# Performance work log

Measured on AMD Instinct MI355X. Metric: run time of the kernel, lower is better.

Reference implementation:

```python
import jax, jax.numpy as jnp
import numpy as np
import jax.ops

N = 100000   # nodes
E = 3200000  # edges
B = 256      # graphs in batch
F_IN, H, C = 128, 64, 2


def gcn_conv(x, src, dst, W, b):
    # PyG GCNConv: x' = D^{-1/2} (A + I) D^{-1/2} (x W) + b
    n = x.shape[0]
    h = x @ W  # [N, H]
    loop = jnp.arange(n)
    s = jnp.concatenate([src, loop])  # add self-loops
    d = jnp.concatenate([dst, loop])
    deg = jax.ops.segment_sum(jnp.ones_like(d, dtype=h.dtype), d, num_segments=n)
    dinv = jnp.where(deg > 0, jax.lax.rsqrt(deg), 0.0)
    norm = dinv[s] * dinv[d]  # [E+N]
    msg = h[s] * norm[:, None]  # gather + scale
    out = jax.ops.segment_sum(msg, d, num_segments=n)  # scatter-add
    return out + b


def setup_inputs() -> dict:
    key = jax.random.key(0)
    ks = jax.random.split(key, 10)
    x = jax.random.normal(ks[0], (N, F_IN), dtype=jnp.float32)
    edge_index = jax.random.randint(ks[1], (2, E), 0, N, dtype=jnp.int64)
    batch = jnp.sort(jax.random.randint(ks[2], (N,), 0, B, dtype=jnp.int64))
    glorot = lambda k, fi, fo: jax.random.uniform(k, (fi, fo), jnp.float32, -1, 1) * np.sqrt(6.0 / (fi + fo))
    return {
        "x": x, "edge_index": edge_index, "batch": batch,
        "W1": glorot(ks[3], F_IN, H), "b1": jnp.zeros((H,), jnp.float32),
        "W2": glorot(ks[4], H, H), "b2": jnp.zeros((H,), jnp.float32),
        "Wl": glorot(ks[5], H, C), "bl": jnp.zeros((C,), jnp.float32),
    }


def reference(x, edge_index, batch, W1, b1, W2, b2, Wl, bl):
    src, dst = edge_index[0], edge_index[1]
    h = jax.nn.relu(gcn_conv(x, src, dst, W1, b1))
    h = jax.nn.relu(gcn_conv(h, src, dst, W2, b2))
    # global_mean_pool over graph ids
    sums = jax.ops.segment_sum(h, batch, num_segments=B)
    cnt = jax.ops.segment_sum(jnp.ones((h.shape[0],), h.dtype), batch, num_segments=B)
    pooled = sums / jnp.maximum(cnt, 1.0)[:, None]  # [B, H]
    return pooled @ Wl + bl  # [B, C]
```

## Files before the change

### kernel.cpp

```cpp
#include <hip/hip_runtime.h>
#include <hip/hip_bf16.h>


#define HDIM 64
#define NB 256
#define SGRID 256

typedef __attribute__((ext_vector_type(8))) short short8;
typedef __attribute__((ext_vector_type(4))) float f32x4;
union FragU { uint4 u; short8 s; };

static __device__ __forceinline__ unsigned bf16_bits(float f) {
    unsigned u = __float_as_uint(f);
    return (u + 0x7fff + ((u >> 16) & 1)) >> 16;
}
static __device__ __forceinline__ float bflo(unsigned w) { return __uint_as_float(w << 16); }
static __device__ __forceinline__ float bfhi(unsigned w) { return __uint_as_float(w & 0xffff0000u); }


__global__ __launch_bounds__(1024) void k_bcount(const int* __restrict__ dst,
        int* __restrict__ blkhist, int E, int npb, int chunk) {
    __shared__ int lh[NB];
    int tid = threadIdx.x;
    if (tid < NB) lh[tid] = 0;
    __syncthreads();
    int e0 = blockIdx.x * chunk, e1 = min(E, e0 + chunk);
    for (int e = e0 + tid; e < e1; e += 1024)
        atomicAdd(&lh[(unsigned)dst[e] / (unsigned)npb], 1);
    __syncthreads();
    if (tid < NB) blkhist[blockIdx.x * NB + tid] = lh[tid];
}

__global__ void k_bscan2(int* __restrict__ blkhist, int* __restrict__ bcnt) {
    __shared__ int s[SGRID];
    int b = blockIdx.x, t = threadIdx.x;
    int orig = blkhist[t * NB + b];
    s[t] = orig;
    __syncthreads();
    for (int off = 1; off < SGRID; off <<= 1) {
        int v = 0;
        if (t >= off) v = s[t - off];
        __syncthreads();
        s[t] += v;
        __syncthreads();
    }
    blkhist[t * NB + b] = s[t] - orig;
    if (t == SGRID - 1) bcnt[b] = s[t];
}

__global__ void k_bscan(const int* __restrict__ bcnt, int* __restrict__ bstart) {
    __shared__ int s[NB];
    int t = threadIdx.x;
    int orig = bcnt[t];
    s[t] = orig;
    __syncthreads();
    for (int off = 1; off < NB; off <<= 1) {
        int v = 0;
        if (t >= off) v = s[t - off];
        __syncthreads();
        s[t] += v;
        __syncthreads();
    }
    bstart[t] = s[t] - orig;
    if (t == NB - 1) bstart[NB] = s[t];
}

__global__ __launch_bounds__(1024) void k_bscatter(const int* __restrict__ src,
        const int* __restrict__ dst, const int* __restrict__ bstart,
        const int* __restrict__ blkhist, unsigned* __restrict__ ebuf,
        int E, int npb, int chunk) {
    __shared__ int base[NB], lcur[NB];
    int tid = threadIdx.x;
    if (tid < NB) {
        base[tid] = bstart[tid] + blkhist[blockIdx.x * NB + tid];
        lcur[tid] = 0;
    }
    __syncthreads();
    int e0 = blockIdx.x * chunk, e1 = min(E, e0 + chunk);
    for (int e = e0 + tid; e < e1; e += 1024) {
        int d = dst[e];
        unsigned b = (unsigned)d / (unsigned)npb;
        unsigned ld = (unsigned)d - b * (unsigned)npb;
        int off = atomicAdd(&lcur[b], 1);
        ebuf[base[b] + off] = (ld << 17) | (unsigned)src[e];
    }
}

__global__ __launch_bounds__(1024) void k_bfill(const unsigned* __restrict__ ebuf,
        const int* __restrict__ bstart, int* __restrict__ row_start,
        int* __restrict__ cnt8, float* __restrict__ dinv, int* __restrict__ csr,
        int N, int npb) {
    __shared__ int h[512], p[512], c[512];
    int b = blockIdx.x, tid = threadIdx.x;
    int vlo = b * npb;
    int vcnt = min(npb, N - vlo);
    if (vcnt <= 0) return;
    for (int i = tid; i < 512; i += 1024) h[i] = 0;
    __syncthreads();
    int e0 = bstart[b], e1 = bstart[b + 1];
    for (int e = e0 + tid; e < e1; e += 1024)
        atomicAdd(&h[ebuf[e] >> 17], 1);
    __syncthreads();
    int pc = 0;
    if (tid < 512) {
        pc = (tid < vcnt) ? ((h[tid] + 7) & ~7) : 0;
        p[tid] = pc;
    }
    __syncthreads();
    for (int off = 1; off < 512; off <<= 1) {
        int v = 0;
        if (tid < 512 && tid >= off) v = p[tid - off];
        __syncthreads();
        if (tid < 512) p[tid] += v;
        __syncthreads();
    }
    int bb = e0 + 7 * vlo;
    if (tid < vcnt) {
        int excl = p[tid] - pc;
        int v = vlo + tid;
        row_start[v] = bb + excl;
        cnt8[v] = pc >> 3;
        dinv[v] = rsqrtf((float)(h[tid] + 1));
        c[tid] = excl;
    }
    __syncthreads();
    for (int e = e0 + tid; e < e1; e += 1024) {
        unsigned ed = ebuf[e];
        int off = atomicAdd(&c[ed >> 17], 1);
        csr[bb + off] = (int)(ed & 0x1FFFFu);
    }
    __syncthreads();
    if (tid < vcnt) {
        int excl = p[tid] - pc;
        for (int q = excl + h[tid]; q < excl + pc; ++q) csr[bb + q] = N;
    }
}

__global__ void k_prep(const float* __restrict__ W1, const float* __restrict__ W2,
                       uint4* __restrict__ W1s, uint4* __restrict__ W2s,
                       unsigned* __restrict__ hsbA, unsigned* __restrict__ hsbB, int N) {
    int t = threadIdx.x;
    int lane = t & 63, ci = t >> 6;
    {
        int kt = ci >> 2, nt = ci & 3;
        int kbase = kt * 32 + (lane >> 4) * 8;
        int n = nt * 16 + (lane & 15);
        uint4 o;
        unsigned* op = (unsigned*)&o;
        for (int jj = 0; jj < 4; ++jj) {
            unsigned lo = bf16_bits(W1[(kbase + 2 * jj) * 64 + n]);
            unsigned hi = bf16_bits(W1[(kbase + 2 * jj + 1) * 64 + n]);
            op[jj] = lo | (hi << 16);
        }
        W1s[ci * 64 + lane] = o;
    }
    if (ci < 8) {
        int kt = ci >> 2, nt = ci & 3;
        int kbase = kt * 32 + (lane >> 4) * 8;
        int n = nt * 16 + (lane & 15);
        uint4 o;
        unsigned* op = (unsigned*)&o;
        for (int jj = 0; jj < 4; ++jj) {
            unsigned lo = bf16_bits(W2[(kbase + 2 * jj) * 64 + n]);
            unsigned hi = bf16_bits(W2[(kbase + 2 * jj + 1) * 64 + n]);
            op[jj] = lo | (hi << 16);
        }
        W2s[ci * 64 + lane] = o;
    }
    if (t < 32) hsbA[(size_t)N * 32 + t] = 0;
    else if (t < 64) hsbB[(size_t)N * 32 + (t - 32)] = 0;
}

#define MFMA_EPILOGUE(OUT)                                                     \
    {                                                                          \
        int col = lane & 15;                                                   \
        float dv[4];                                                           \
        for (int r = 0; r < 4; ++r) {                                          \
            int vr = v0 + quad * 4 + r;                                        \
            dv[r] = dinv[vr < n ? vr : (n - 1)];                               \
        }                                                                      \
        for (int nt = 0; nt < 4; ++nt)                                         \
            for (int r = 0; r < 4; ++r) {                                      \
                int vr = v0 + quad * 4 + r;                                    \
                float val = acc[nt][r] * dv[r];                                \
                float oth = __shfl_xor(val, 1, 64);                            \
                if (!(lane & 1) && vr < n)                                     \
                    OUT[(size_t)vr * 32 + nt * 8 + (col >> 1)] =               \
                        bf16_bits(val) | (bf16_bits(oth) << 16);               \
            }                                                                  \
    }

__global__ __launch_bounds__(256) void k_mgemm1(const float* __restrict__ X,
        const uint4* __restrict__ W1s, const float* __restrict__ dinv,
        unsigned* __restrict__ hsb, int n) {
    int lane = threadIdx.x & 63, wv = threadIdx.x >> 6;
    int v0 = (blockIdx.x * 4 + wv) * 16;
    if (v0 >= n) return;
    int quad = lane >> 4;
    int vm = v0 + (lane & 15); if (vm >= n) vm = n - 1;
    const float* xr = X + (size_t)vm * 128 + quad * 8;
    f32x4 acc[4] = {f32x4{0,0,0,0}, f32x4{0,0,0,0}, f32x4{0,0,0,0}, f32x4{0,0,0,0}};
#pragma unroll
    for (int kt = 0; kt < 4; ++kt) {
        float4 xa = *(const float4*)(xr + kt * 32);
        float4 xb = *(const float4*)(xr + kt * 32 + 4);
        FragU a;
        a.u.x = bf16_bits(xa.x) | (bf16_bits(xa.y) << 16);
        a.u.y = bf16_bits(xa.z) | (bf16_bits(xa.w) << 16);
        a.u.z = bf16_bits(xb.x) | (bf16_bits(xb.y) << 16);
        a.u.w = bf16_bits(xb.z) | (bf16_bits(xb.w) << 16);
#pragma unroll
        for (int nt = 0; nt < 4; ++nt) {
            FragU b; b.u = W1s[(kt * 4 + nt) * 64 + lane];
            acc[nt] = __builtin_amdgcn_mfma_f32_16x16x32_bf16(a.s, b.s, acc[nt], 0, 0, 0);
        }
    }
    MFMA_EPILOGUE(hsb)
}

__global__ __launch_bounds__(256) void k_mgemm2(const unsigned* __restrict__ h1b,
        const uint4* __restrict__ W2s, const float* __restrict__ dinv,
        unsigned* __restrict__ hsbB, int n) {
    int lane = threadIdx.x & 63, wv = threadIdx.x >> 6;
    int v0 = (blockIdx.x * 4 + wv) * 16;
    if (v0 >= n) return;
    int quad = lane >> 4;
    int vm = v0 + (lane & 15); if (vm >= n) vm = n - 1;
    const uint4* h4 = (const uint4*)h1b;
    f32x4 acc[4] = {f32x4{0,0,0,0}, f32x4{0,0,0,0}, f32x4{0,0,0,0}, f32x4{0,0,0,0}};
#pragma unroll
    for (int kt = 0; kt < 2; ++kt) {
        FragU a; a.u = h4[(size_t)vm * 8 + kt * 4 + quad];
#pragma unroll
        for (int nt = 0; nt < 4; ++nt) {
            FragU b; b.u = W2s[(kt * 4 + nt) * 64 + lane];
            acc[nt] = __builtin_amdgcn_mfma_f32_16x16x32_bf16(a.s, b.s, acc[nt], 0, 0, 0);
        }
    }
    MFMA_EPILOGUE(hsbB)
}

#define GATHER_BODY                                                            \
    const uint4* hs4p = (const uint4*)hsb;                                     \
    int o = lane & 7, oct = lane >> 3;                                         \
    float a0=0.f,a1=0.f,a2=0.f,a3=0.f,a4=0.f,a5=0.f,a6=0.f,a7=0.f;             \
    if (oct == 0) {                                                            \
        uint4 s = hs4p[(size_t)v * 8 + o];                                     \
        a0=bflo(s.x);a1=bfhi(s.x);a2=bflo(s.y);a3=bfhi(s.y);                   \
        a4=bflo(s.z);a5=bfhi(s.z);a6=bflo(s.w);a7=bfhi(s.w);                   \
    }                                                                          \
    int rs = row_start[v], nb = cnt8[v];                                       \
    for (int base = 0; base < nb; base += 8) {                                 \
        int idx = csr[rs + base * 8 + lane];   \
        int m = nb - base; if (m > 8) m = 8;                 \
        uint4 wb[8];                                                           \
        _Pragma("unroll")                                                      \
        for (int i = 0; i < 8; ++i)                                            \
            if (i < m) {                                                       \
                int u = __shfl(idx, i * 8 + oct, 64);                          \
                wb[i] = hs4p[(size_t)u * 8 + o];                               \
            }                                                                  \
        _Pragma("unroll")                                                      \
        for (int i = 0; i < 8; ++i)                                            \
            if (i < m) {                                                       \
                a0+=bflo(wb[i].x);a1+=bfhi(wb[i].x);                           \
                a2+=bflo(wb[i].y);a3+=bfhi(wb[i].y);                           \
                a4+=bflo(wb[i].z);a5+=bfhi(wb[i].z);                           \
                a6+=bflo(wb[i].w);a7+=bfhi(wb[i].w);                           \
            }                                                                  \
    }                                                                          \
    a0+=__shfl_xor(a0,8,64);a0+=__shfl_xor(a0,16,64);a0+=__shfl_xor(a0,32,64); \
    a1+=__shfl_xor(a1,8,64);a1+=__shfl_xor(a1,16,64);a1+=__shfl_xor(a1,32,64); \
    a2+=__shfl_xor(a2,8,64);a2+=__shfl_xor(a2,16,64);a2+=__shfl_xor(a2,32,64); \
    a3+=__shfl_xor(a3,8,64);a3+=__shfl_xor(a3,16,64);a3+=__shfl_xor(a3,32,64); \
    a4+=__shfl_xor(a4,8,64);a4+=__shfl_xor(a4,16,64);a4+=__shfl_xor(a4,32,64); \
    a5+=__shfl_xor(a5,8,64);a5+=__shfl_xor(a5,16,64);a5+=__shfl_xor(a5,32,64); \
    a6+=__shfl_xor(a6,8,64);a6+=__shfl_xor(a6,16,64);a6+=__shfl_xor(a6,32,64); \
    a7+=__shfl_xor(a7,8,64);a7+=__shfl_xor(a7,16,64);a7+=__shfl_xor(a7,32,64); \
    float dv = dinv[v];                                                        \
    float4 bb0 = ((const float4*)bias)[2 * o];                                 \
    float4 bb1 = ((const float4*)bias)[2 * o + 1];                             \
    float r0 = fmaxf(fmaf(dv, a0, bb0.x), 0.f);                                \
    float r1 = fmaxf(fmaf(dv, a1, bb0.y), 0.f);                                \
    float r2 = fmaxf(fmaf(dv, a2, bb0.z), 0.f);                                \
    float r3 = fmaxf(fmaf(dv, a3, bb0.w), 0.f);                                \
    float r4 = fmaxf(fmaf(dv, a4, bb1.x), 0.f);                                \
    float r5 = fmaxf(fmaf(dv, a5, bb1.y), 0.f);                                \
    float r6 = fmaxf(fmaf(dv, a6, bb1.z), 0.f);                                \
    float r7 = fmaxf(fmaf(dv, a7, bb1.w), 0.f);

__global__ void k_conv1(const unsigned* __restrict__ hsb, const int* __restrict__ row_start,
                        const int* __restrict__ cnt8, const int* __restrict__ csr,
                        const float* __restrict__ dinv, const float* __restrict__ bias,
                        unsigned* __restrict__ h1b, int n) {
    int v = (blockIdx.x * 256 + threadIdx.x) >> 6;
    int lane = threadIdx.x & 63;
    if (v >= n) return;
    GATHER_BODY
    if (oct == 0) {
        uint4 pk;
        pk.x = bf16_bits(r0) | (bf16_bits(r1) << 16);
        pk.y = bf16_bits(r2) | (bf16_bits(r3) << 16);
        pk.z = bf16_bits(r4) | (bf16_bits(r5) << 16);
        pk.w = bf16_bits(r6) | (bf16_bits(r7) << 16);
        ((uint4*)h1b)[(size_t)v * 8 + o] = pk;
    }
}

__global__ void k_conv_out(const unsigned* __restrict__ hsb, const int* __restrict__ row_start,
                           const int* __restrict__ cnt8, const int* __restrict__ csr,
                           const float* __restrict__ dinv, const float* __restrict__ bias,
                           const float* __restrict__ Wl, float2* __restrict__ z, int n) {
    int v = (blockIdx.x * 256 + threadIdx.x) >> 6;
    int lane = threadIdx.x & 63;
    if (v >= n) return;
    GATHER_BODY
    const float4* Wl4 = (const float4*)Wl;
    float4 wA = Wl4[4 * o + 0];
    float4 wB = Wl4[4 * o + 1];
    float4 wC = Wl4[4 * o + 2];
    float4 wD = Wl4[4 * o + 3];
    float c0 = r0*wA.x + r1*wA.z + r2*wB.x + r3*wB.z + r4*wC.x + r5*wC.z + r6*wD.x + r7*wD.z;
    float c1 = r0*wA.y + r1*wA.w + r2*wB.y + r3*wB.w + r4*wC.y + r5*wC.w + r6*wD.y + r7*wD.w;
    c0 += __shfl_xor(c0, 1, 64); c1 += __shfl_xor(c1, 1, 64);
    c0 += __shfl_xor(c0, 2, 64); c1 += __shfl_xor(c1, 2, 64);
    c0 += __shfl_xor(c0, 4, 64); c1 += __shfl_xor(c1, 4, 64);
    if (lane == 0) z[v] = make_float2(c0, c1);
}

static __device__ __forceinline__ int lower_bound(const int* __restrict__ a, int n, int key) {
    int lo = 0, hi = n;
    while (lo < hi) {
        int mid = (lo + hi) >> 1;
        if (a[mid] < key) lo = mid + 1; else hi = mid;
    }
    return lo;
}

__global__ void k_pool_z(const float2* __restrict__ z, const int* __restrict__ batch,
                         const float* __restrict__ bl, float* __restrict__ out, int N, int B) {
    int g = (blockIdx.x * 256 + threadIdx.x) >> 6;
    int lane = threadIdx.x & 63;
    if (g >= B) return;
    int lo = lower_bound(batch, N, g);
    int hi = lower_bound(batch, N, g + 1);
    float c0 = 0.f, c1 = 0.f;
    for (int v = lo + lane; v < hi; v += 64) {
        float2 t = z[v];
        c0 += t.x; c1 += t.y;
    }
    #pragma unroll
    for (int off = 32; off; off >>= 1) {
        c0 += __shfl_xor(c0, off, 64);
        c1 += __shfl_xor(c1, off, 64);
    }
    if (lane == 0) {
        float inv = 1.0f / fmaxf((float)(hi - lo), 1.0f);
        out[g * 2 + 0] = c0 * inv + bl[0];
        out[g * 2 + 1] = c1 * inv + bl[1];
    }
}

extern "C" void kernel_launch(void* const* d_in, const int* in_sizes, int n_in,
                              void* d_out, int out_size, void* d_ws, size_t ws_size,
                              hipStream_t stream) {
    const float* x  = (const float*)d_in[0];
    const int* edge = (const int*)d_in[1];
    const int* batch= (const int*)d_in[2];
    const float* W1 = (const float*)d_in[3];
    const float* b1 = (const float*)d_in[4];
    const float* W2 = (const float*)d_in[5];
    const float* b2 = (const float*)d_in[6];
    const float* Wl = (const float*)d_in[7];
    const float* bl = (const float*)d_in[8];
    float* out = (float*)d_out;

    const int N = in_sizes[2];
    const int E = in_sizes[1] / 2;
    const int B = out_size / 2;
    const int* srcp = edge;
    const int* dstp = edge + E;
    const int npb = (N + NB - 1) / NB;

    char* w = (char*)d_ws;
    auto carve = [&](size_t bytes) { void* p = (void*)w; w += (bytes + 255) & ~(size_t)255; return p; };
    int*      cnt8    = (int*)carve((size_t)N * 4);
    int*      rsA     = (int*)carve((size_t)N * 4);
    float*    dinv    = (float*)carve((size_t)N * 4);
    int*      bcnt    = (int*)carve((NB + 8) * 4);
    int*      bstart  = (int*)carve((NB + 8) * 4);
    int*      blkhist = (int*)carve((size_t)SGRID * NB * 4);
    uint4*    W1s     = (uint4*)carve(16 * 64 * 16);
    uint4*    W2s     = (uint4*)carve(8 * 64 * 16);
    int*      csr     = (int*)carve(((size_t)E + 7 * (size_t)N + 256) * 4);
    unsigned* hsbA    = (unsigned*)carve(((size_t)N + 1) * 32 * 4);
    unsigned* ebuf    = hsbA;
    unsigned* h1b     = (unsigned*)carve(((size_t)N + 1) * 32 * 4);
    unsigned* hsbB    = (unsigned*)carve(((size_t)N + 1) * 32 * 4);
    float2*   zbuf    = (float2*)carve((size_t)N * 8);

    const int chunk = (E + SGRID - 1) / SGRID;
    int wbl = (N + 3) / 4;
    int gbl = (N + 63) / 64;

    k_bcount<<<SGRID, 1024, 0, stream>>>(dstp, blkhist, E, npb, chunk);
    k_bscan2<<<NB, SGRID, 0, stream>>>(blkhist, bcnt);
    k_bscan<<<1, NB, 0, stream>>>(bcnt, bstart);
    k_bscatter<<<SGRID, 1024, 0, stream>>>(srcp, dstp, bstart, blkhist, ebuf, E, npb, chunk);
    k_bfill<<<NB, 1024, 0, stream>>>(ebuf, bstart, rsA, cnt8, dinv, csr, N, npb);
    k_prep<<<1, 1024, 0, stream>>>(W1, W2, W1s, W2s, hsbA, hsbB, N);

    k_mgemm1<<<gbl, 256, 0, stream>>>(x, W1s, dinv, hsbA, N);
    k_conv1<<<wbl, 256, 0, stream>>>(hsbA, rsA, cnt8, csr, dinv, b1, h1b, N);
    k_mgemm2<<<gbl, 256, 0, stream>>>(h1b, W2s, dinv, hsbB, N);
    k_conv_out<<<wbl, 256, 0, stream>>>(hsbB, rsA, cnt8, csr, dinv, b2, Wl, zbuf, N);

    k_pool_z<<<(B * 64 + 255) / 256, 256, 0, stream>>>(zbuf, batch, bl, out, N, B);
}
```

Measured before the change: 324.9 us.

## Fuse bucket scan with weight prep, stage X in LDS, restructure gather loop

```diff
diff --git a/kernel.cpp b/kernel.cpp
--- a/kernel.cpp
+++ b/kernel.cpp
@@ -8,6 +8,7 @@
 
 typedef __attribute__((ext_vector_type(8))) short short8;
 typedef __attribute__((ext_vector_type(4))) float f32x4;
+typedef __attribute__((ext_vector_type(2))) float f32x2;
 union FragU { uint4 u; short8 s; };
 
 static __device__ __forceinline__ unsigned bf16_bits(float f) {
@@ -48,98 +49,24 @@
     if (t == SGRID - 1) bcnt[b] = s[t];
 }
 
-__global__ void k_bscan(const int* __restrict__ bcnt, int* __restrict__ bstart) {
+__global__ __launch_bounds__(1024) void k_bscan_prep(const int* __restrict__ bcnt,
+        int* __restrict__ bstart, const float* __restrict__ W1,
+        const float* __restrict__ W2, uint4* __restrict__ W1s, uint4* __restrict__ W2s,
+        unsigned* __restrict__ hsbA, unsigned* __restrict__ hsbB, int N) {
     __shared__ int s[NB];
     int t = threadIdx.x;
-    int orig = bcnt[t];
-    s[t] = orig;
+    int orig = 0;
+    if (t < NB) { orig = bcnt[t]; s[t] = orig; }
     __syncthreads();
     for (int off = 1; off < NB; off <<= 1) {
         int v = 0;
-        if (t >= off) v = s[t - off];
-        __syncthreads();
-        s[t] += v;
-        __syncthreads();
-    }
-    bstart[t] = s[t] - orig;
+        if (t < NB && t >= off) v = s[t - off];
+        __syncthreads();
+        if (t < NB) s[t] += v;
+        __syncthreads();
+    }
+    if (t < NB) bstart[t] = s[t] - orig;
     if (t == NB - 1) bstart[NB] = s[t];
-}
-
-__global__ __launch_bounds__(1024) void k_bscatter(const int* __restrict__ src,
-        const int* __restrict__ dst, const int* __restrict__ bstart,
-        const int* __restrict__ blkhist, unsigned* __restrict__ ebuf,
-        int E, int npb, int chunk) {
-    __shared__ int base[NB], lcur[NB];
-    int tid = threadIdx.x;
-    if (tid < NB) {
-        base[tid] = bstart[tid] + blkhist[blockIdx.x * NB + tid];
-        lcur[tid] = 0;
-    }
-    __syncthreads();
-    int e0 = blockIdx.x * chunk, e1 = min(E, e0 + chunk);
-    for (int e = e0 + tid; e < e1; e += 1024) {
-        int d = dst[e];
-        unsigned b = (unsigned)d / (unsigned)npb;
-        unsigned ld = (unsigned)d - b * (unsigned)npb;
-        int off = atomicAdd(&lcur[b], 1);
-        ebuf[base[b] + off] = (ld << 17) | (unsigned)src[e];
-    }
-}
-
-__global__ __launch_bounds__(1024) void k_bfill(const unsigned* __restrict__ ebuf,
-        const int* __restrict__ bstart, int* __restrict__ row_start,
-        int* __restrict__ cnt8, float* __restrict__ dinv, int* __restrict__ csr,
-        int N, int npb) {
-    __shared__ int h[512], p[512], c[512];
-    int b = blockIdx.x, tid = threadIdx.x;
-    int vlo = b * npb;
-    int vcnt = min(npb, N - vlo);
-    if (vcnt <= 0) return;
-    for (int i = tid; i < 512; i += 1024) h[i] = 0;
-    __syncthreads();
-    int e0 = bstart[b], e1 = bstart[b + 1];
-    for (int e = e0 + tid; e < e1; e += 1024)
-        atomicAdd(&h[ebuf[e] >> 17], 1);
-    __syncthreads();
-    int pc = 0;
-    if (tid < 512) {
-        pc = (tid < vcnt) ? ((h[tid] + 7) & ~7) : 0;
-        p[tid] = pc;
-    }
-    __syncthreads();
-    for (int off = 1; off < 512; off <<= 1) {
-        int v = 0;
-        if (tid < 512 && tid >= off) v = p[tid - off];
-        __syncthreads();
-        if (tid < 512) p[tid] += v;
-        __syncthreads();
-    }
-    int bb = e0 + 7 * vlo;
-    if (tid < vcnt) {
-        int excl = p[tid] - pc;
-        int v = vlo + tid;
-        row_start[v] = bb + excl;
-        cnt8[v] = pc >> 3;
-        dinv[v] = rsqrtf((float)(h[tid] + 1));
-        c[tid] = excl;
-    }
-    __syncthreads();
-    for (int e = e0 + tid; e < e1; e += 1024) {
-        unsigned ed = ebuf[e];
-        int off = atomicAdd(&c[ed >> 17], 1);
-        csr[bb + off] = (int)(ed & 0x1FFFFu);
-    }
-    __syncthreads();
-    if (tid < vcnt) {
-        int excl = p[tid] - pc;
-        for (int q = excl + h[tid]; q < excl + pc; ++q) csr[bb + q] = N;
-    }
-}
-
-__global__ void k_prep(const float* __restrict__ W1, const float* __restrict__ W2,
-                       uint4* __restrict__ W1s, uint4* __restrict__ W2s,
-                       unsigned* __restrict__ hsbA, unsigned* __restrict__ hsbB, int N) {
-    int t = threadIdx.x;
     int lane = t & 63, ci = t >> 6;
     {
         int kt = ci >> 2, nt = ci & 3;
@@ -169,6 +96,77 @@
     }
     if (t < 32) hsbA[(size_t)N * 32 + t] = 0;
     else if (t < 64) hsbB[(size_t)N * 32 + (t - 32)] = 0;
+}
+
+__global__ __launch_bounds__(1024) void k_bscatter(const int* __restrict__ src,
+        const int* __restrict__ dst, const int* __restrict__ bstart,
+        const int* __restrict__ blkhist, unsigned* __restrict__ ebuf,
+        int E, int npb, int chunk) {
+    __shared__ int base[NB], lcur[NB];
+    int tid = threadIdx.x;
+    if (tid < NB) {
+        base[tid] = bstart[tid] + blkhist[blockIdx.x * NB + tid];
+        lcur[tid] = 0;
+    }
+    __syncthreads();
+    int e0 = blockIdx.x * chunk, e1 = min(E, e0 + chunk);
+    for (int e = e0 + tid; e < e1; e += 1024) {
+        int d = dst[e];
+        unsigned b = (unsigned)d / (unsigned)npb;
+        unsigned ld = (unsigned)d - b * (unsigned)npb;
+        int off = atomicAdd(&lcur[b], 1);
+        ebuf[base[b] + off] = (ld << 17) | (unsigned)src[e];
+    }
+}
+
+__global__ __launch_bounds__(1024) void k_bfill(const unsigned* __restrict__ ebuf,
+        const int* __restrict__ bstart, int* __restrict__ row_start,
+        int* __restrict__ cnt8, float* __restrict__ dinv, int* __restrict__ csr,
+        int N, int npb) {
+    __shared__ int h[512], p[512], c[512];
+    int b = blockIdx.x, tid = threadIdx.x;
+    int vlo = b * npb;
+    int vcnt = min(npb, N - vlo);
+    if (vcnt <= 0) return;
+    for (int i = tid; i < 512; i += 1024) h[i] = 0;
+    __syncthreads();
+    int e0 = bstart[b], e1 = bstart[b + 1];
+    for (int e = e0 + tid; e < e1; e += 1024)
+        atomicAdd(&h[ebuf[e] >> 17], 1);
+    __syncthreads();
+    int pc = 0;
+    if (tid < 512) {
+        pc = (tid < vcnt) ? ((h[tid] + 7) & ~7) : 0;
+        p[tid] = pc;
+    }
+    __syncthreads();
+    for (int off = 1; off < 512; off <<= 1) {
+        int v = 0;
+        if (tid < 512 && tid >= off) v = p[tid - off];
+        __syncthreads();
+        if (tid < 512) p[tid] += v;
+        __syncthreads();
+    }
+    int bb = e0 + 7 * vlo;
+    if (tid < vcnt) {
+        int excl = p[tid] - pc;
+        int v = vlo + tid;
+        row_start[v] = bb + excl;
+        cnt8[v] = pc >> 3;
+        dinv[v] = rsqrtf((float)(h[tid] + 1));
+        c[tid] = excl;
+    }
+    __syncthreads();
+    for (int e = e0 + tid; e < e1; e += 1024) {
+        unsigned ed = ebuf[e];
+        int off = atomicAdd(&c[ed >> 17], 1);
+        csr[bb + off] = (int)(ed & 0x1FFFFu);
+    }
+    __syncthreads();
+    if (tid < vcnt) {
+        int excl = p[tid] - pc;
+        for (int q = excl + h[tid]; q < excl + pc; ++q) csr[bb + q] = N;
+    }
 }
 
 #define MFMA_EPILOGUE(OUT)                                                     \
@@ -193,12 +191,21 @@
 __global__ __launch_bounds__(256) void k_mgemm1(const float* __restrict__ X,
         const uint4* __restrict__ W1s, const float* __restrict__ dinv,
         unsigned* __restrict__ hsb, int n) {
+    __shared__ float Xs[4][16 * 132];
     int lane = threadIdx.x & 63, wv = threadIdx.x >> 6;
     int v0 = (blockIdx.x * 4 + wv) * 16;
     if (v0 >= n) return;
+    const float4* X4 = (const float4*)X;
+#pragma unroll
+    for (int i = 0; i < 8; ++i) {
+        int gi = i * 64 + lane;
+        int r = gi >> 5, c4 = gi & 31;
+        int vr = v0 + r; if (vr >= n) vr = n - 1;
+        float4 t = X4[(size_t)vr * 32 + c4];
+        *(float4*)&Xs[wv][r * 132 + c4 * 4] = t;
+    }
     int quad = lane >> 4;
-    int vm = v0 + (lane & 15); if (vm >= n) vm = n - 1;
-    const float* xr = X + (size_t)vm * 128 + quad * 8;
+    const float* xr = &Xs[wv][(lane & 15) * 132 + quad * 8];
     f32x4 acc[4] = {f32x4{0,0,0,0}, f32x4{0,0,0,0}, f32x4{0,0,0,0}, f32x4{0,0,0,0}};
 #pragma unroll
     for (int kt = 0; kt < 4; ++kt) {
@@ -240,59 +247,57 @@
     MFMA_EPILOGUE(hsbB)
 }
 
+#define RED2(A)                                                                \
+    A.x += __shfl_xor(A.x, 8, 64); A.x += __shfl_xor(A.x, 16, 64);             \
+    A.x += __shfl_xor(A.x, 32, 64);                                            \
+    A.y += __shfl_xor(A.y, 8, 64); A.y += __shfl_xor(A.y, 16, 64);             \
+    A.y += __shfl_xor(A.y, 32, 64);
+
 #define GATHER_BODY                                                            \
     const uint4* hs4p = (const uint4*)hsb;                                     \
     int o = lane & 7, oct = lane >> 3;                                         \
-    float a0=0.f,a1=0.f,a2=0.f,a3=0.f,a4=0.f,a5=0.f,a6=0.f,a7=0.f;             \
+    f32x2 A0 = {0.f,0.f}, A1 = {0.f,0.f}, A2 = {0.f,0.f}, A3 = {0.f,0.f};      \
     if (oct == 0) {                                                            \
         uint4 s = hs4p[(size_t)v * 8 + o];                                     \
-        a0=bflo(s.x);a1=bfhi(s.x);a2=bflo(s.y);a3=bfhi(s.y);                   \
-        a4=bflo(s.z);a5=bfhi(s.z);a6=bflo(s.w);a7=bfhi(s.w);                   \
+        A0 = (f32x2){bflo(s.x), bfhi(s.x)};                                    \
+        A1 = (f32x2){bflo(s.y), bfhi(s.y)};                                    \
+        A2 = (f32x2){bflo(s.z), bfhi(s.z)};                                    \
+        A3 = (f32x2){bflo(s.w), bfhi(s.w)};                                    \
     }                                                                          \
     int rs = row_start[v], nb = cnt8[v];                                       \
+    const int* cp = csr + rs + oct;                                            \
     for (int base = 0; base < nb; base += 8) {                                 \
-        int idx = csr[rs + base * 8 + lane];   \
         int m = nb - base; if (m > 8) m = 8;                 \
-        uint4 wb[8];                                                           \
+        int u[8]; uint4 wb[8];                                                 \
         _Pragma("unroll")                                                      \
-        for (int i = 0; i < 8; ++i)                                            \
-            if (i < m) {                                                       \
-                int u = __shfl(idx, i * 8 + oct, 64);                          \
-                wb[i] = hs4p[(size_t)u * 8 + o];                               \
-            }                                                                  \
+        for (int i = 0; i < 8; ++i) if (i < m) u[i] = cp[(base + i) * 8];      \
         _Pragma("unroll")                                                      \
-        for (int i = 0; i < 8; ++i)                                            \
-            if (i < m) {                                                       \
-                a0+=bflo(wb[i].x);a1+=bfhi(wb[i].x);                           \
-                a2+=bflo(wb[i].y);a3+=bfhi(wb[i].y);                           \
-                a4+=bflo(wb[i].z);a5+=bfhi(wb[i].z);                           \
-                a6+=bflo(wb[i].w);a7+=bfhi(wb[i].w);                           \
-            }                                                                  \
+        for (int i = 0; i < 8; ++i) if (i < m) wb[i] = hs4p[(size_t)u[i] * 8 + o]; \
+        _Pragma("unroll")                                                      \
+        for (int i = 0; i < 8; ++i) if (i < m) {                               \
+            A0 += (f32x2){bflo(wb[i].x), bfhi(wb[i].x)};                       \
+            A1 += (f32x2){bflo(wb[i].y), bfhi(wb[i].y)};                       \
+            A2 += (f32x2){bflo(wb[i].z), bfhi(wb[i].z)};                       \
+            A3 += (f32x2){bflo(wb[i].w), bfhi(wb[i].w)};                       \
+        }                                                                      \
     }                                                                          \
-    a0+=__shfl_xor(a0,8,64);a0+=__shfl_xor(a0,16,64);a0+=__shfl_xor(a0,32,64); \
-    a1+=__shfl_xor(a1,8,64);a1+=__shfl_xor(a1,16,64);a1+=__shfl_xor(a1,32,64); \
-    a2+=__shfl_xor(a2,8,64);a2+=__shfl_xor(a2,16,64);a2+=__shfl_xor(a2,32,64); \
-    a3+=__shfl_xor(a3,8,64);a3+=__shfl_xor(a3,16,64);a3+=__shfl_xor(a3,32,64); \
-    a4+=__shfl_xor(a4,8,64);a4+=__shfl_xor(a4,16,64);a4+=__shfl_xor(a4,32,64); \
-    a5+=__shfl_xor(a5,8,64);a5+=__shfl_xor(a5,16,64);a5+=__shfl_xor(a5,32,64); \
-    a6+=__shfl_xor(a6,8,64);a6+=__shfl_xor(a6,16,64);a6+=__shfl_xor(a6,32,64); \
-    a7+=__shfl_xor(a7,8,64);a7+=__shfl_xor(a7,16,64);a7+=__shfl_xor(a7,32,64); \
+    RED2(A0) RED2(A1) RED2(A2) RED2(A3)                                        \
     float dv = dinv[v];                                                        \
     float4 bb0 = ((const float4*)bias)[2 * o];                                 \
     float4 bb1 = ((const float4*)bias)[2 * o + 1];                             \
-    float r0 = fmaxf(fmaf(dv, a0, bb0.x), 0.f);                                \
-    float r1 = fmaxf(fmaf(dv, a1, bb0.y), 0.f);                                \
-    float r2 = fmaxf(fmaf(dv, a2, bb0.z), 0.f);                                \
-    float r3 = fmaxf(fmaf(dv, a3, bb0.w), 0.f);                                \
-    float r4 = fmaxf(fmaf(dv, a4, bb1.x), 0.f);                                \
-    float r5 = fmaxf(fmaf(dv, a5, bb1.y), 0.f);                                \
-    float r6 = fmaxf(fmaf(dv, a6, bb1.z), 0.f);                                \
-    float r7 = fmaxf(fmaf(dv, a7, bb1.w), 0.f);
-
-__global__ void k_conv1(const unsigned* __restrict__ hsb, const int* __restrict__ row_start,
-                        const int* __restrict__ cnt8, const int* __restrict__ csr,
-                        const float* __restrict__ dinv, const float* __restrict__ bias,
-                        unsigned* __restrict__ h1b, int n) {
+    float r0 = fmaxf(fmaf(dv, A0.x, bb0.x), 0.f);                              \
+    float r1 = fmaxf(fmaf(dv, A0.y, bb0.y), 0.f);                              \
+    float r2 = fmaxf(fmaf(dv, A1.x, bb0.z), 0.f);                              \
+    float r3 = fmaxf(fmaf(dv, A1.y, bb0.w), 0.f);                              \
+    float r4 = fmaxf(fmaf(dv, A2.x, bb1.x), 0.f);                              \
+    float r5 = fmaxf(fmaf(dv, A2.y, bb1.y), 0.f);                              \
+    float r6 = fmaxf(fmaf(dv, A3.x, bb1.z), 0.f);                              \
+    float r7 = fmaxf(fmaf(dv, A3.y, bb1.w), 0.f);
+
+__global__ __launch_bounds__(256, 6) void k_conv1(const unsigned* __restrict__ hsb,
+        const int* __restrict__ row_start, const int* __restrict__ cnt8,
+        const int* __restrict__ csr, const float* __restrict__ dinv,
+        const float* __restrict__ bias, unsigned* __restrict__ h1b, int n) {
     int v = (blockIdx.x * 256 + threadIdx.x) >> 6;
     int lane = threadIdx.x & 63;
     if (v >= n) return;
@@ -307,10 +312,11 @@
     }
 }
 
-__global__ void k_conv_out(const unsigned* __restrict__ hsb, const int* __restrict__ row_start,
-                           const int* __restrict__ cnt8, const int* __restrict__ csr,
-                           const float* __restrict__ dinv, const float* __restrict__ bias,
-                           const float* __restrict__ Wl, float2* __restrict__ z, int n) {
+__global__ __launch_bounds__(256, 6) void k_conv_out(const unsigned* __restrict__ hsb,
+        const int* __restrict__ row_start, const int* __restrict__ cnt8,
+        const int* __restrict__ csr, const float* __restrict__ dinv,
+        const float* __restrict__ bias, const float* __restrict__ Wl,
+        float2* __restrict__ z, int n) {
     int v = (blockIdx.x * 256 + threadIdx.x) >> 6;
     int lane = threadIdx.x & 63;
     if (v >= n) return;
@@ -405,10 +411,9 @@
 
     k_bcount<<<SGRID, 1024, 0, stream>>>(dstp, blkhist, E, npb, chunk);
     k_bscan2<<<NB, SGRID, 0, stream>>>(blkhist, bcnt);
-    k_bscan<<<1, NB, 0, stream>>>(bcnt, bstart);
+    k_bscan_prep<<<1, 1024, 0, stream>>>(bcnt, bstart, W1, W2, W1s, W2s, hsbA, hsbB, N);
     k_bscatter<<<SGRID, 1024, 0, stream>>>(srcp, dstp, bstart, blkhist, ebuf, E, npb, chunk);
     k_bfill<<<NB, 1024, 0, stream>>>(ebuf, bstart, rsA, cnt8, dinv, csr, N, npb);
-    k_prep<<<1, 1024, 0, stream>>>(W1, W2, W1s, W2s, hsbA, hsbB, N);
 
     k_mgemm1<<<gbl, 256, 0, stream>>>(x, W1s, dinv, hsbA, N);
     k_conv1<<<wbl, 256, 0, stream>>>(hsbA, rsA, cnt8, csr, dinv, b1, h1b, N);
```

After: 358.7 us. 10.4% more time.
